# Optimization experiments

Measured on AMD Instinct MI355X. Metric: run time of the kernel, lower is better.

## Reference

```python
import jax, jax.numpy as jnp
import numpy as np

H = 1024      # hidden_size
V = 50257     # output_size (vocab)
L = 4096      # encoder sequence length


def setup_inputs() -> dict:
    key = jax.random.key(0)
    ks = jax.random.split(key, 14)
    s = 0.02  # param init scale
    return {
        "y_before": jax.random.randint(ks[0], (1,), 0, V),
        "s_before": jax.random.normal(ks[1], (1, 1, H), jnp.float32),
        "h_all": jax.random.normal(ks[2], (L, H), jnp.float32),
        # parameters
        "emb_W": jax.random.normal(ks[3], (V, H), jnp.float32) * s,
        "align_W": jax.random.normal(ks[4], (1, 2 * H), jnp.float32) * s,
        "align_b": jax.random.normal(ks[5], (1,), jnp.float32) * s,
        "new_W": jax.random.normal(ks[6], (H, 2 * H), jnp.float32) * s,
        "new_b": jax.random.normal(ks[7], (H,), jnp.float32) * s,
        "W_ih": jax.random.normal(ks[8], (3 * H, H), jnp.float32) * s,
        "b_ih": jax.random.normal(ks[9], (3 * H,), jnp.float32) * s,
        "W_hh": jax.random.normal(ks[10], (3 * H, H), jnp.float32) * s,
        "b_hh": jax.random.normal(ks[11], (3 * H,), jnp.float32) * s,
        "out_W": jax.random.normal(ks[12], (V, H), jnp.float32) * s,
        "out_b": jax.random.normal(ks[13], (V,), jnp.float32) * s,
    }


def reference(y_before, s_before, h_all, emb_W, align_W, align_b,
              new_W, new_b, W_ih, b_ih, W_hh, b_hh, out_W, out_b):
    # embedding lookup; dropout is identity at inference
    emb = emb_W[y_before[0]]                      # [H]
    s_prev = s_before[0, 0]                       # [H]

    # additive attention scores: Linear([h; s]) split into h-part and s-part
    Wh = align_W[0, :H]                           # [H]
    Ws = align_W[0, H:]                           # [H]
    e = h_all @ Wh + (s_prev @ Ws) + align_b[0]   # [L]
    a = jax.nn.softmax(e)                         # [L]
    c = a @ h_all                                 # [H] context

    # new_state linear on cat(emb, context)
    x = jnp.concatenate([emb, c]) @ new_W.T + new_b  # [H]

    # single GRU step (PyTorch gate order: r, z, n)
    gi = W_ih @ x + b_ih                          # [3H]
    gh = W_hh @ s_prev + b_hh                     # [3H]
    i_r, i_z, i_n = jnp.split(gi, 3)
    h_r, h_z, h_n = jnp.split(gh, 3)
    r = jax.nn.sigmoid(i_r + h_r)
    z = jax.nn.sigmoid(i_z + h_z)
    n = jnp.tanh(i_n + r * h_n)
    h_new = (1.0 - z) * n + z * s_prev            # [H]

    logp = jax.nn.log_softmax(h_new @ out_W.T + out_b)  # [V]
    return logp[None, :], h_new[None, None, :], a[None, :]
```

## Files before the change

### kernel.cpp

```cpp
#include <hip/hip_runtime.h>
#include <math.h>

#define H 1024
#define V 50257
#define L 4096
#define LOGITS_BLOCKS ((V + 15) / 16)

__device__ __forceinline__ float wave_sum(float v) {
    #pragma unroll
    for (int off = 32; off; off >>= 1) v += __shfl_down(v, off);
    return v;
}

__device__ __forceinline__ void lse_merge(float& m, float& s, float m2, float s2) {
    if (m2 == -INFINITY) return;
    if (m == -INFINITY) { m = m2; s = s2; return; }
    float nm = fmaxf(m, m2);
    s = s * expf(m - nm) + s2 * expf(m2 - nm);
    m = nm;
}

__global__ void k_scores(const float* __restrict__ h_all, const float* __restrict__ s_prev,
                         const float* __restrict__ align_W, const float* __restrict__ align_b,
                         float* __restrict__ e) {
    int wave = threadIdx.x >> 6, lane = threadIdx.x & 63;
    int l = blockIdx.x * 4 + wave;
    const float* hrow = h_all + (size_t)l * H;
    const float* Wh = align_W;
    const float* Ws = align_W + H;
    float acc = 0.f;
    #pragma unroll
    for (int it = 0; it < 4; ++it) {
        int k = it * 256 + lane * 4;
        float4 h4 = *(const float4*)(hrow + k);
        float4 w4 = *(const float4*)(Wh + k);
        float4 s4 = *(const float4*)(s_prev + k);
        float4 v4 = *(const float4*)(Ws + k);
        acc += h4.x * w4.x + h4.y * w4.y + h4.z * w4.z + h4.w * w4.w;
        acc += s4.x * v4.x + s4.y * v4.y + s4.z * v4.z + s4.w * v4.w;
    }
    acc = wave_sum(acc);
    if (lane == 0) e[l] = acc + align_b[0];
}

__global__ void k_softmax(const float* __restrict__ e, float* __restrict__ a_ws,
                          float* __restrict__ a_out, float* __restrict__ c_ws) {
    __shared__ float redm[16];
    __shared__ float reds[16];
    int tid = threadIdx.x;
    int lane = tid & 63, wave = tid >> 6;
    c_ws[tid] = 0.f;
    float v[4];
    float m = -INFINITY;
    #pragma unroll
    for (int i = 0; i < 4; ++i) { v[i] = e[tid + i * 1024]; m = fmaxf(m, v[i]); }
    #pragma unroll
    for (int off = 32; off; off >>= 1) m = fmaxf(m, __shfl_down(m, off));
    if (lane == 0) redm[wave] = m;
    __syncthreads();
    if (tid == 0) {
        float mm = redm[0];
        for (int w = 1; w < 16; ++w) mm = fmaxf(mm, redm[w]);
        redm[0] = mm;
    }
    __syncthreads();
    m = redm[0];
    float s = 0.f;
    #pragma unroll
    for (int i = 0; i < 4; ++i) { v[i] = expf(v[i] - m); s += v[i]; }
    s = wave_sum(s);
    if (lane == 0) reds[wave] = s;
    __syncthreads();
    if (tid == 0) {
        float ss = 0.f;
        for (int w = 0; w < 16; ++w) ss += reds[w];
        reds[0] = ss;
    }
    __syncthreads();
    float inv = 1.f / reds[0];
    #pragma unroll
    for (int i = 0; i < 4; ++i) {
        float av = v[i] * inv;
        a_ws[tid + i * 1024] = av;
        a_out[tid + i * 1024] = av;
    }
}

__global__ void k_context(const float* __restrict__ h_all, const float* __restrict__ a,
                          float* __restrict__ c) {
    int j = threadIdx.x;
    int l0 = blockIdx.x * 16;
    float acc = 0.f;
    #pragma unroll
    for (int l = l0; l < l0 + 16; ++l)
        acc += a[l] * h_all[(size_t)l * H + j];
    atomicAdd(c + j, acc);
}

__global__ void k_xvec(const float* __restrict__ new_W, const float* __restrict__ new_b,
                       const float* __restrict__ emb_W, const int* __restrict__ y,
                       const float* __restrict__ c, float* __restrict__ x) {
    int wave = threadIdx.x >> 6, lane = threadIdx.x & 63;
    int i = blockIdx.x * 4 + wave;
    const float* row = new_W + (size_t)i * (2 * H);
    const float* emb = emb_W + (size_t)y[0] * H;
    float acc = 0.f;
    #pragma unroll
    for (int it = 0; it < 8; ++it) {
        int k = it * 256 + lane * 4;
        float4 w4 = *(const float4*)(row + k);
        float4 v4 = (k < H) ? *(const float4*)(emb + k) : *(const float4*)(c + (k - H));
        acc += w4.x * v4.x + w4.y * v4.y + w4.z * v4.z + w4.w * v4.w;
    }
    acc = wave_sum(acc);
    if (lane == 0) x[i] = acc + new_b[i];
}

__global__ void k_gru(const float* __restrict__ W_ih, const float* __restrict__ b_ih,
                      const float* __restrict__ W_hh, const float* __restrict__ b_hh,
                      const float* __restrict__ x, const float* __restrict__ s_prev,
                      float* __restrict__ h_ws, float* __restrict__ h_out) {
    __shared__ float dots[6];
    int wave = threadIdx.x >> 6, lane = threadIdx.x & 63;
    int i = blockIdx.x;
    int g = wave % 3;
    const float* row;
    const float* vec;
    if (wave < 3) { row = W_ih + (size_t)(g * H + i) * H; vec = x; }
    else          { row = W_hh + (size_t)(g * H + i) * H; vec = s_prev; }
    float acc = 0.f;
    #pragma unroll
    for (int it = 0; it < 4; ++it) {
        int k = it * 256 + lane * 4;
        float4 w4 = *(const float4*)(row + k);
        float4 v4 = *(const float4*)(vec + k);
        acc += w4.x * v4.x + w4.y * v4.y + w4.z * v4.z + w4.w * v4.w;
    }
    acc = wave_sum(acc);
    if (lane == 0) dots[wave] = acc;
    __syncthreads();
    if (threadIdx.x == 0) {
        float ir  = dots[0] + b_ih[i];
        float iz  = dots[1] + b_ih[H + i];
        float in_ = dots[2] + b_ih[2 * H + i];
        float hr  = dots[3] + b_hh[i];
        float hz  = dots[4] + b_hh[H + i];
        float hn  = dots[5] + b_hh[2 * H + i];
        float r = 1.f / (1.f + expf(-(ir + hr)));
        float z = 1.f / (1.f + expf(-(iz + hz)));
        float n = tanhf(in_ + r * hn);
        float h = (1.f - z) * n + z * s_prev[i];
        h_ws[i]  = h;
        h_out[i] = h;
    }
}

__global__ void k_logits(const float* __restrict__ out_W, const float* __restrict__ out_b,
                         const float* __restrict__ h, float* __restrict__ logits,
                         float2* __restrict__ pairs) {
    __shared__ float sh_h[H];
    __shared__ float2 wpair[4];
    for (int k = threadIdx.x; k < H; k += 256) sh_h[k] = h[k];
    __syncthreads();
    int wave = threadIdx.x >> 6, lane = threadIdx.x & 63;
    float m = -INFINITY, s = 0.f;
    #pragma unroll
    for (int rr = 0; rr < 4; ++rr) {
        int v = blockIdx.x * 16 + wave * 4 + rr;
        if (v >= V) continue;
        const float* row = out_W + (size_t)v * H;
        float acc = 0.f;
        #pragma unroll
        for (int it = 0; it < 4; ++it) {
            int k = it * 256 + lane * 4;
            float4 w4 = *(const float4*)(row + k);
            float4 h4 = *(const float4*)(sh_h + k);
            acc += w4.x * h4.x + w4.y * h4.y + w4.z * h4.z + w4.w * h4.w;
        }
        acc = wave_sum(acc);
        if (lane == 0) {
            float logit = acc + out_b[v];
            logits[v] = logit;
            lse_merge(m, s, logit, 1.0f);
        }
    }
    if (lane == 0) wpair[wave] = make_float2(m, s);
    __syncthreads();
    if (threadIdx.x == 0) {
        float M = wpair[0].x, S = wpair[0].y;
        for (int w = 1; w < 4; ++w) lse_merge(M, S, wpair[w].x, wpair[w].y);
        pairs[blockIdx.x] = make_float2(M, S);
    }
}

__global__ void k_combine(const float2* __restrict__ pairs, int n, float* __restrict__ ms) {
    __shared__ float redm[16];
    __shared__ float reds[16];
    int tid = threadIdx.x, lane = tid & 63, wave = tid >> 6;
    float m = -INFINITY, s = 0.f;
    for (int i = tid; i < n; i += 1024) {
        float2 p = pairs[i];
        lse_merge(m, s, p.x, p.y);
    }
    #pragma unroll
    for (int off = 32; off; off >>= 1) {
        float m2 = __shfl_down(m, off);
        float s2 = __shfl_down(s, off);
        lse_merge(m, s, m2, s2);
    }
    if (lane == 0) { redm[wave] = m; reds[wave] = s; }
    __syncthreads();
    if (tid == 0) {
        float M = redm[0], S = reds[0];
        for (int w = 1; w < 16; ++w) lse_merge(M, S, redm[w], reds[w]);
        ms[0] = M;
        ms[1] = logf(S);
    }
}

__global__ void k_finalize(float* __restrict__ logits, const float* __restrict__ ms) {
    int v = blockIdx.x * 256 + threadIdx.x;
    if (v < V) logits[v] = logits[v] - ms[0] - ms[1];
}

extern "C" void kernel_launch(void* const* d_in, const int* in_sizes, int n_in,
                              void* d_out, int out_size, void* d_ws, size_t ws_size,
                              hipStream_t stream) {
    const int*   y       = (const int*)d_in[0];
    const float* s_prev  = (const float*)d_in[1];
    const float* h_all   = (const float*)d_in[2];
    const float* emb_W   = (const float*)d_in[3];
    const float* align_W = (const float*)d_in[4];
    const float* align_b = (const float*)d_in[5];
    const float* new_W   = (const float*)d_in[6];
    const float* new_b   = (const float*)d_in[7];
    const float* W_ih    = (const float*)d_in[8];
    const float* b_ih    = (const float*)d_in[9];
    const float* W_hh    = (const float*)d_in[10];
    const float* b_hh    = (const float*)d_in[11];
    const float* out_W   = (const float*)d_in[12];
    const float* out_b   = (const float*)d_in[13];

    float* out      = (float*)d_out;
    float* logp_out = out;
    float* h_out    = out + V;
    float* a_out    = out + V + H;

    float*  ws       = (float*)d_ws;
    float*  ws_e     = ws;
    float*  ws_a     = ws + 4096;
    float*  ws_c     = ws + 8192;
    float*  ws_x     = ws + 9216;
    float*  ws_h     = ws + 10240;
    float*  ws_ms    = ws + 11264;
    float2* ws_pairs = (float2*)(ws + 11266);

    k_scores  <<<L / 4, 256, 0, stream>>>(h_all, s_prev, align_W, align_b, ws_e);
    k_softmax <<<1, 1024, 0, stream>>>(ws_e, ws_a, a_out, ws_c);
    k_context <<<L / 16, 1024, 0, stream>>>(h_all, ws_a, ws_c);
    k_xvec    <<<H / 4, 256, 0, stream>>>(new_W, new_b, emb_W, y, ws_c, ws_x);
    k_gru     <<<H, 384, 0, stream>>>(W_ih, b_ih, W_hh, b_hh, ws_x, s_prev, ws_h, h_out);
    k_logits  <<<LOGITS_BLOCKS, 256, 0, stream>>>(out_W, out_b, ws_h, logp_out, ws_pairs);
    k_combine <<<1, 1024, 0, stream>>>(ws_pairs, LOGITS_BLOCKS, ws_ms);
    k_finalize<<<(V + 255) / 256, 256, 0, stream>>>(logp_out, ws_ms);
}
```

Measured before the change: 443.1 us.

## Fuse attention into online-softmax split kernels and multi-row logits GEMV

Replaces the scores/softmax/context chain with a split-softmax scheme. Each block computes 16 scores, a local max and sum, and a partial context vector. A merge kernel then rescales and reduces these, which removes the single-block softmax and the atomics. The logits kernel now computes 8 rows per wave to raise memory-level parallelism, and the LSE combine is folded into the finalize kernel, so every finalize block redundantly reduces all pairs. These changes cut launches and serial single-block stages, at the cost of extra partial-context traffic (256xH floats) and repeated pair reductions.

```diff
diff --git a/kernel.cpp b/kernel.cpp
--- a/kernel.cpp
+++ b/kernel.cpp
@@ -4,7 +4,9 @@
 #define H 1024
 #define V 50257
 #define L 4096
-#define LOGITS_BLOCKS ((V + 15) / 16)
+#define NB_ATTN 256
+#define ROWS_PER_LOGB 32
+#define LOGITS_BLOCKS ((V + ROWS_PER_LOGB - 1) / ROWS_PER_LOGB)
 
 __device__ __forceinline__ float wave_sum(float v) {
     #pragma unroll
@@ -20,11 +22,16 @@
     m = nm;
 }
 
-__global__ void k_scores(const float* __restrict__ h_all, const float* __restrict__ s_prev,
-                         const float* __restrict__ align_W, const float* __restrict__ align_b,
-                         float* __restrict__ e) {
-    int wave = threadIdx.x >> 6, lane = threadIdx.x & 63;
-    int l = blockIdx.x * 4 + wave;
+__global__ __launch_bounds__(1024) void k_attn(
+    const float* __restrict__ h_all, const float* __restrict__ s_prev,
+    const float* __restrict__ align_W, const float* __restrict__ align_b,
+    float* __restrict__ p_ws, float2* __restrict__ pairs,
+    float* __restrict__ cpart) {
+    __shared__ float sh_e[16];
+    __shared__ float sh_p[16];
+    int tid = threadIdx.x, wave = tid >> 6, lane = tid & 63;
+    int b = blockIdx.x;
+    int l = b * 16 + wave;
     const float* hrow = h_all + (size_t)l * H;
     const float* Wh = align_W;
     const float* Ws = align_W + H;
@@ -40,61 +47,72 @@
         acc += s4.x * v4.x + s4.y * v4.y + s4.z * v4.z + s4.w * v4.w;
     }
     acc = wave_sum(acc);
-    if (lane == 0) e[l] = acc + align_b[0];
-}
-
-__global__ void k_softmax(const float* __restrict__ e, float* __restrict__ a_ws,
-                          float* __restrict__ a_out, float* __restrict__ c_ws) {
-    __shared__ float redm[16];
-    __shared__ float reds[16];
-    int tid = threadIdx.x;
-    int lane = tid & 63, wave = tid >> 6;
-    c_ws[tid] = 0.f;
-    float v[4];
-    float m = -INFINITY;
-    #pragma unroll
-    for (int i = 0; i < 4; ++i) { v[i] = e[tid + i * 1024]; m = fmaxf(m, v[i]); }
-    #pragma unroll
-    for (int off = 32; off; off >>= 1) m = fmaxf(m, __shfl_down(m, off));
-    if (lane == 0) redm[wave] = m;
-    __syncthreads();
-    if (tid == 0) {
-        float mm = redm[0];
-        for (int w = 1; w < 16; ++w) mm = fmaxf(mm, redm[w]);
-        redm[0] = mm;
-    }
-    __syncthreads();
-    m = redm[0];
-    float s = 0.f;
-    #pragma unroll
-    for (int i = 0; i < 4; ++i) { v[i] = expf(v[i] - m); s += v[i]; }
-    s = wave_sum(s);
-    if (lane == 0) reds[wave] = s;
-    __syncthreads();
-    if (tid == 0) {
-        float ss = 0.f;
-        for (int w = 0; w < 16; ++w) ss += reds[w];
-        reds[0] = ss;
-    }
-    __syncthreads();
-    float inv = 1.f / reds[0];
-    #pragma unroll
-    for (int i = 0; i < 4; ++i) {
-        float av = v[i] * inv;
-        a_ws[tid + i * 1024] = av;
-        a_out[tid + i * 1024] = av;
-    }
-}
-
-__global__ void k_context(const float* __restrict__ h_all, const float* __restrict__ a,
-                          float* __restrict__ c) {
-    int j = threadIdx.x;
-    int l0 = blockIdx.x * 16;
-    float acc = 0.f;
-    #pragma unroll
-    for (int l = l0; l < l0 + 16; ++l)
-        acc += a[l] * h_all[(size_t)l * H + j];
-    atomicAdd(c + j, acc);
+    if (lane == 0) sh_e[wave] = acc + align_b[0];
+    __syncthreads();
+    float m_b = sh_e[0];
+    #pragma unroll
+    for (int i = 1; i < 16; ++i) m_b = fmaxf(m_b, sh_e[i]);
+    if (tid < 16) {
+        float p = expf(sh_e[tid] - m_b);
+        sh_p[tid] = p;
+        p_ws[b * 16 + tid] = p;
+    }
+    __syncthreads();
+    if (tid == 0) {
+        float s_b = 0.f;
+        #pragma unroll
+        for (int i = 0; i < 16; ++i) s_b += sh_p[i];
+        pairs[b] = make_float2(m_b, s_b);
+    }
+    float cacc = 0.f;
+    #pragma unroll
+    for (int i = 0; i < 16; ++i)
+        cacc += sh_p[i] * h_all[(size_t)(b * 16 + i) * H + tid];
+    cpart[(size_t)b * H + tid] = cacc;
+}
+
+__global__ __launch_bounds__(1024) void k_merge(
+    const float2* __restrict__ pairs, const float* __restrict__ p_ws,
+    const float* __restrict__ cpart, float* __restrict__ a_out,
+    float* __restrict__ c) {
+    __shared__ float shm[16], shs[16];
+    __shared__ float shMS[2];
+    __shared__ float shc4[16];
+    int tid = threadIdx.x, wave = tid >> 6, lane = tid & 63;
+    float m = -INFINITY, s = 0.f;
+    if (tid < NB_ATTN) { float2 pr = pairs[tid]; m = pr.x; s = pr.y; }
+    #pragma unroll
+    for (int off = 32; off; off >>= 1) {
+        float m2 = __shfl_down(m, off);
+        float s2 = __shfl_down(s, off);
+        lse_merge(m, s, m2, s2);
+    }
+    if (lane == 0) { shm[wave] = m; shs[wave] = s; }
+    __syncthreads();
+    if (tid == 0) {
+        float M = shm[0], S = shs[0];
+        for (int w = 1; w < 16; ++w) lse_merge(M, S, shm[w], shs[w]);
+        shMS[0] = M; shMS[1] = S;
+    }
+    __syncthreads();
+    float M = shMS[0];
+    float invS = 1.f / shMS[1];
+    if (tid < 16) {
+        float scale = expf(pairs[blockIdx.x].x - M) * invS;
+        a_out[blockIdx.x * 16 + tid] = p_ws[blockIdx.x * 16 + tid] * scale;
+    }
+    int cl = tid >> 8;
+    int r  = tid & 255;
+    int col = blockIdx.x * 4 + cl;
+    float w_r = expf(pairs[r].x - M);
+    float val = w_r * cpart[(size_t)r * H + col];
+    val = wave_sum(val);
+    if (lane == 0) shc4[wave] = val;
+    __syncthreads();
+    if (tid < 4) {
+        float sum = shc4[tid * 4] + shc4[tid * 4 + 1] + shc4[tid * 4 + 2] + shc4[tid * 4 + 3];
+        c[blockIdx.x * 4 + tid] = sum * invS;
+    }
 }
 
 __global__ void k_xvec(const float* __restrict__ new_W, const float* __restrict__ new_b,
@@ -155,52 +173,69 @@
     }
 }
 
-__global__ void k_logits(const float* __restrict__ out_W, const float* __restrict__ out_b,
-                         const float* __restrict__ h, float* __restrict__ logits,
-                         float2* __restrict__ pairs) {
-    __shared__ float sh_h[H];
+__global__ __launch_bounds__(256, 4) void k_logits(
+    const float* __restrict__ out_W, const float* __restrict__ out_b,
+    const float* __restrict__ h, float* __restrict__ logits,
+    float2* __restrict__ pairs) {
+    __shared__ __align__(16) float sh_h[H];
     __shared__ float2 wpair[4];
-    for (int k = threadIdx.x; k < H; k += 256) sh_h[k] = h[k];
-    __syncthreads();
-    int wave = threadIdx.x >> 6, lane = threadIdx.x & 63;
-    float m = -INFINITY, s = 0.f;
-    #pragma unroll
-    for (int rr = 0; rr < 4; ++rr) {
-        int v = blockIdx.x * 16 + wave * 4 + rr;
-        if (v >= V) continue;
-        const float* row = out_W + (size_t)v * H;
-        float acc = 0.f;
+    int tid = threadIdx.x, wave = tid >> 6, lane = tid & 63;
+    ((float4*)sh_h)[tid] = ((const float4*)h)[tid];
+    __syncthreads();
+    int v0 = blockIdx.x * ROWS_PER_LOGB + wave * 8;
+    const float* base = out_W + (size_t)v0 * H;
+    float acc[8] = {0.f, 0.f, 0.f, 0.f, 0.f, 0.f, 0.f, 0.f};
+    if (v0 + 8 <= V) {
         #pragma unroll
         for (int it = 0; it < 4; ++it) {
             int k = it * 256 + lane * 4;
-            float4 w4 = *(const float4*)(row + k);
             float4 h4 = *(const float4*)(sh_h + k);
-            acc += w4.x * h4.x + w4.y * h4.y + w4.z * h4.z + w4.w * h4.w;
+            #pragma unroll
+            for (int r = 0; r < 8; ++r) {
+                float4 w4 = *(const float4*)(base + (size_t)r * H + k);
+                acc[r] += w4.x * h4.x + w4.y * h4.y + w4.z * h4.z + w4.w * h4.w;
+            }
         }
-        acc = wave_sum(acc);
-        if (lane == 0) {
-            float logit = acc + out_b[v];
-            logits[v] = logit;
+    } else {
+        for (int r = 0; r < 8; ++r) {
+            if (v0 + r >= V) break;
+            const float* rowp = base + (size_t)r * H;
+            #pragma unroll
+            for (int it = 0; it < 4; ++it) {
+                int k = it * 256 + lane * 4;
+                float4 h4 = *(const float4*)(sh_h + k);
+                float4 w4 = *(const float4*)(rowp + k);
+                acc[r] += w4.x * h4.x + w4.y * h4.y + w4.z * h4.z + w4.w * h4.w;
+            }
+        }
+    }
+    float m = -INFINITY, s = 0.f;
+    #pragma unroll
+    for (int r = 0; r < 8; ++r) {
+        float red = wave_sum(acc[r]);
+        if (lane == 0 && v0 + r < V) {
+            float logit = red + out_b[v0 + r];
+            logits[v0 + r] = logit;
             lse_merge(m, s, logit, 1.0f);
         }
     }
     if (lane == 0) wpair[wave] = make_float2(m, s);
     __syncthreads();
-    if (threadIdx.x == 0) {
+    if (tid == 0) {
         float M = wpair[0].x, S = wpair[0].y;
         for (int w = 1; w < 4; ++w) lse_merge(M, S, wpair[w].x, wpair[w].y);
         pairs[blockIdx.x] = make_float2(M, S);
     }
 }
 
-__global__ void k_combine(const float2* __restrict__ pairs, int n, float* __restrict__ ms) {
-    __shared__ float redm[16];
-    __shared__ float reds[16];
-    int tid = threadIdx.x, lane = tid & 63, wave = tid >> 6;
+__global__ void k_final(const float2* __restrict__ pairs, float* __restrict__ logits) {
+    __shared__ float shm[4], shs[4];
+    __shared__ float shMS[2];
+    int tid = threadIdx.x, wave = tid >> 6, lane = tid & 63;
     float m = -INFINITY, s = 0.f;
-    for (int i = tid; i < n; i += 1024) {
-        float2 p = pairs[i];
-        lse_merge(m, s, p.x, p.y);
+    for (int i = tid; i < LOGITS_BLOCKS; i += 256) {
+        float2 pr = pairs[i];
+        lse_merge(m, s, pr.x, pr.y);
     }
     #pragma unroll
     for (int off = 32; off; off >>= 1) {
@@ -208,19 +243,16 @@
         float s2 = __shfl_down(s, off);
         lse_merge(m, s, m2, s2);
     }
-    if (lane == 0) { redm[wave] = m; reds[wave] = s; }
-    __syncthreads();
-    if (tid == 0) {
-        float M = redm[0], S = reds[0];
-        for (int w = 1; w < 16; ++w) lse_merge(M, S, redm[w], reds[w]);
-        ms[0] = M;
-        ms[1] = logf(S);
-    }
-}
-
-__global__ void k_finalize(float* __restrict__ logits, const float* __restrict__ ms) {
-    int v = blockIdx.x * 256 + threadIdx.x;
-    if (v < V) logits[v] = logits[v] - ms[0] - ms[1];
+    if (lane == 0) { shm[wave] = m; shs[wave] = s; }
+    __syncthreads();
+    if (tid == 0) {
+        float M = shm[0], S = shs[0];
+        for (int w = 1; w < 4; ++w) lse_merge(M, S, shm[w], shs[w]);
+        shMS[0] = M; shMS[1] = logf(S);
+    }
+    __syncthreads();
+    int v = blockIdx.x * 256 + tid;
+    if (v < V) logits[v] = logits[v] - shMS[0] - shMS[1];
 }
 
 extern "C" void kernel_launch(void* const* d_in, const int* in_sizes, int n_in,
@@ -246,21 +278,20 @@
     float* h_out    = out + V;
     float* a_out    = out + V + H;
 
-    float*  ws       = (float*)d_ws;
-    float*  ws_e     = ws;
-    float*  ws_a     = ws + 4096;
-    float*  ws_c     = ws + 8192;
-    float*  ws_x     = ws + 9216;
-    float*  ws_h     = ws + 10240;
-    float*  ws_ms    = ws + 11264;
-    float2* ws_pairs = (float2*)(ws + 11266);
-
-    k_scores  <<<L / 4, 256, 0, stream>>>(h_all, s_prev, align_W, align_b, ws_e);
-    k_softmax <<<1, 1024, 0, stream>>>(ws_e, ws_a, a_out, ws_c);
-    k_context <<<L / 16, 1024, 0, stream>>>(h_all, ws_a, ws_c);
-    k_xvec    <<<H / 4, 256, 0, stream>>>(new_W, new_b, emb_W, y, ws_c, ws_x);
-    k_gru     <<<H, 384, 0, stream>>>(W_ih, b_ih, W_hh, b_hh, ws_x, s_prev, ws_h, h_out);
-    k_logits  <<<LOGITS_BLOCKS, 256, 0, stream>>>(out_W, out_b, ws_h, logp_out, ws_pairs);
-    k_combine <<<1, 1024, 0, stream>>>(ws_pairs, LOGITS_BLOCKS, ws_ms);
-    k_finalize<<<(V + 255) / 256, 256, 0, stream>>>(logp_out, ws_ms);
-}
+    float*  ws      = (float*)d_ws;
+    float*  ws_p    = ws;
+    float2* ws_pr1  = (float2*)(ws + 4096);
+    float*  ws_cp   = ws + 4096 + 512;
+    float*  ws_c    = ws_cp + (size_t)NB_ATTN * H;
+    float*  ws_x    = ws_c + H;
+    float*  ws_h    = ws_x + H;
+    float2* ws_pr2  = (float2*)(ws_h + H);
+
+    k_attn  <<<NB_ATTN, 1024, 0, stream>>>(h_all, s_prev, align_W, align_b,
+                                           ws_p, ws_pr1, ws_cp);
+    k_merge <<<NB_ATTN, 1024, 0, stream>>>(ws_pr1, ws_p, ws_cp, a_out, ws_c);
+    k_xvec  <<<H / 4, 256, 0, stream>>>(new_W, new_b, emb_W, y, ws_c, ws_x);
+    k_gru   <<<H, 384, 0, stream>>>(W_ih, b_ih, W_hh, b_hh, ws_x, s_prev, ws_h, h_out);
+    k_logits<<<LOGITS_BLOCKS, 256, 0, stream>>>(out_W, out_b, ws_h, logp_out, ws_pr2);
+    k_final <<<(V + 255) / 256, 256, 0, stream>>>(ws_pr2, logp_out);
+}
```

After: 438.4 us. Within noise of the previous version (-1.0%).
